# Optimization experiments

Hardware: AMD Instinct MI355X
Metric: run time of the kernel (lower is better)

Reference implementation:

```python
import jax, jax.numpy as jnp
import numpy as np

VALUE_RANGE = 16
D_MODEL = 1024
NUM_TILES = 8
NUM_FREQS = 6
BATCH = 65536
TEMPERATURE = 0.5


def _fourier(x):
    # x: (B,) -> (B, 2*NUM_FREQS); freqs = 2**[0..F)
    freqs = 2.0 ** jnp.arange(NUM_FREQS, dtype=jnp.float32)
    ang = x[:, None] * (2.0 * np.pi / VALUE_RANGE) * freqs[None, :]
    return jnp.concatenate([jnp.sin(ang), jnp.cos(ang)], axis=-1)


def _layernorm(x, g, b, eps=1e-5):
    m = jnp.mean(x, axis=-1, keepdims=True)
    v = jnp.var(x, axis=-1, keepdims=True)
    return (x - m) * jax.lax.rsqrt(v + eps) * g + b


def _gelu(x):
    return jax.nn.gelu(x, approximate=False)  # torch nn.GELU() default is exact erf


def setup_inputs() -> dict:
    key = jax.random.key(0)
    ks = jax.random.split(key, 16)
    d, T, F4 = D_MODEL, NUM_TILES, 4 * NUM_FREQS
    s = lambda i, shape, scale: (jax.random.normal(ks[i], shape, jnp.float32) * scale)
    return {
        "a": jax.random.uniform(ks[0], (BATCH,), jnp.float32, 0.0, float(VALUE_RANGE)),
        "b": jax.random.uniform(ks[1], (BATCH,), jnp.float32, 0.0, float(VALUE_RANGE)),
        "W_in": s(2, (F4, d), 0.05), "b_in": jnp.zeros((d,), jnp.float32),
        "ln_g": jnp.ones((d,), jnp.float32), "ln_b": jnp.zeros((d,), jnp.float32),
        "Wr1_sum": s(3, (d, d), 0.03), "br1_sum": jnp.zeros((d,), jnp.float32),
        "Wr2_sum": s(4, (d, T), 0.03), "br2_sum": jnp.zeros((T,), jnp.float32),
        "Wr1_diff": s(5, (d, d), 0.03), "br1_diff": jnp.zeros((d,), jnp.float32),
        "Wr2_diff": s(6, (d, T), 0.03), "br2_diff": jnp.zeros((T,), jnp.float32),
        "We1": s(7, (T, d, 2 * d), 0.03), "be1": jnp.zeros((T, 2 * d), jnp.float32),
        "We2": s(8, (T, 2 * d, d), 0.02), "be2": jnp.zeros((T, d), jnp.float32),
        "w_sum": s(9, (d,), 0.03), "bs": jnp.zeros((), jnp.float32),
        "w_diff": s(10, (d,), 0.03), "bd": jnp.zeros((), jnp.float32),
    }


def reference(a, b, W_in, b_in, ln_g, ln_b,
              Wr1_sum, br1_sum, Wr2_sum, br2_sum,
              Wr1_diff, br1_diff, Wr2_diff, br2_diff,
              We1, be1, We2, be2, w_sum, bs, w_diff, bd):
    # Shared encoder
    x = jnp.concatenate([_fourier(a), _fourier(b)], axis=-1)      # (B, 4F)
    x = _gelu(_layernorm(x @ W_in + b_in, ln_g, ln_b))            # (B, d)
    # Top-1 routing (temperature scaling does not change argmax, kept for fidelity)
    sum_logits = (_gelu(x @ Wr1_sum + br1_sum) @ Wr2_sum + br2_sum) / TEMPERATURE
    diff_logits = (_gelu(x @ Wr1_diff + br1_diff) @ Wr2_diff + br2_diff) / TEMPERATURE
    sum_tile = jnp.argmax(sum_logits, axis=-1)                    # (B,)
    diff_tile = jnp.argmax(diff_logits, axis=-1)                  # (B,)
    # Expert dispatch: loop over small fixed num_tiles, mask-combine per token.
    sum_hidden = jnp.zeros_like(x)
    diff_hidden = jnp.zeros_like(x)
    for t in range(We1.shape[0]):
        y = _gelu(x @ We1[t] + be1[t]) @ We2[t] + be2[t]          # (B, d)
        sum_hidden = sum_hidden + jnp.where((sum_tile == t)[:, None], y, 0.0)
        diff_hidden = diff_hidden + jnp.where((diff_tile == t)[:, None], y, 0.0)
    sum_pred = sum_hidden @ w_sum + bs                            # (B,)
    diff_pred = diff_hidden @ w_diff + bd                         # (B,)
    return (sum_pred, diff_pred)
```

## Files before the change

### kernel.cpp

```cpp
#include <hip/hip_runtime.h>
#include <math.h>


#define BT 65536
#define QN 65536
#define TSTR QN
#define D 1024
#define NT 8
#define DH 2048
#define RCAP 8192
#define RTOK 8
#define DELTA 0.010f
#define XJCAP 768

typedef _Float16 f16;
typedef _Float16 f16x8 __attribute__((ext_vector_type(8)));
typedef _Float16 f16x4 __attribute__((ext_vector_type(4)));
typedef float f32x16 __attribute__((ext_vector_type(16)));

__device__ __forceinline__ float gelu_f(float v) {
    return 0.5f * v * (1.0f + erff(v * 0.70710678118654752440f));
}

__device__ __forceinline__ float gelu_fast(float x) {
    float ax = fabsf(x) * 0.70710678118654752440f;
    float t = __builtin_amdgcn_rcpf(1.0f + 0.3275911f * ax);
    float p = t * (0.254829592f + t * (-0.284496736f + t * (1.421413741f +
              t * (-1.453152027f + t * 1.061405429f))));
    float er = 1.0f - p * __expf(-ax * ax);
    er = copysignf(er, x);
    return 0.5f * x * (1.0f + er);
}

__device__ __forceinline__ void gload16(const void* g, void* l) {
    __builtin_amdgcn_global_load_lds(
        (const __attribute__((address_space(1))) void*)g,
        (__attribute__((address_space(3))) void*)l, 16, 0, 0);
}

__global__ __launch_bounds__(256) void k_prev(
    const float* __restrict__ We2, const float* __restrict__ w_sum,
    const float* __restrict__ w_diff, const float* __restrict__ be2,
    const float* __restrict__ bs, const float* __restrict__ bd,
    float* __restrict__ v_sum, float* __restrict__ v_diff,
    float* __restrict__ c_sum, float* __restrict__ c_diff)
{
    int bid = blockIdx.x;
    if (bid < 4096) {
        int row  = bid * 4 + (threadIdx.x >> 6);
        int lane = threadIdx.x & 63;
        const float* r = We2 + (size_t)row * D;
        float s1 = 0.f, s2 = 0.f;
        #pragma unroll
        for (int i = 0; i < 4; i++) {
            int o4 = (lane + 64 * i) * 4;
            float4 w = *(const float4*)(r + o4);
            float4 u = *(const float4*)(w_sum + o4);
            float4 v = *(const float4*)(w_diff + o4);
            s1 += w.x*u.x + w.y*u.y + w.z*u.z + w.w*u.w;
            s2 += w.x*v.x + w.y*v.y + w.z*v.z + w.w*v.w;
        }
        #pragma unroll
        for (int m = 32; m >= 1; m >>= 1) {
            s1 += __shfl_xor(s1, m, 64);
            s2 += __shfl_xor(s2, m, 64);
        }
        if (lane == 0) { v_sum[row] = s1; v_diff[row] = s2; }
    } else {
        int t = threadIdx.x;
        if (t < 8) {
            float s = 0.f; const float* r = be2 + t * D;
            for (int k = 0; k < D; k++) s += r[k] * w_sum[k];
            c_sum[t] = s + bs[0];
        } else if (t < 16) {
            int tt = t - 8;
            float s = 0.f; const float* r = be2 + tt * D;
            for (int k = 0; k < D; k++) s += r[k] * w_diff[k];
            c_diff[tt] = s + bd[0];
        }
    }
}

__global__ __launch_bounds__(256) void k_cvt(
    const float* __restrict__ We1, f16* __restrict__ We1T)
{
    __shared__ float tile[64][65];
    int b = blockIdx.x;
    int e = b >> 9, rem = b & 511;
    int kt = rem >> 5, nt = rem & 31;
    int tid = threadIdx.x;
    const float* src = We1 + ((size_t)e * D + kt * 64) * DH + nt * 64;
    #pragma unroll
    for (int i = 0; i < 16; i++) {
        int idx = tid + 256 * i;
        int kk = idx >> 6, nn = idx & 63;
        tile[kk][nn] = src[(size_t)kk * DH + nn];
    }
    __syncthreads();
    f16* dst = We1T + ((size_t)e * DH + nt * 64) * D + kt * 64;
    #pragma unroll
    for (int i = 0; i < 16; i++) {
        int idx = tid + 256 * i;
        int nn = idx >> 6, kk = idx & 63;
        dst[(size_t)nn * D + kk] = (f16)tile[kk][nn];
    }
}

__global__ __launch_bounds__(256) void k_cvtR(
    const float* __restrict__ Wr1s, const float* __restrict__ Wr1d,
    f16* __restrict__ Wr1Tf)
{
    __shared__ float tile[64][65];
    int b = blockIdx.x;
    int z = b >> 8, rem = b & 255;
    int kt = rem >> 4, nt2 = rem & 15;
    int tid = threadIdx.x;
    const float* W = z ? Wr1d : Wr1s;
    const float* src = W + (size_t)(kt * 64) * 1024 + nt2 * 64;
    #pragma unroll
    for (int i = 0; i < 16; i++) {
        int idx = tid + 256 * i;
        int kk = idx >> 6, nn = idx & 63;
        tile[kk][nn] = src[(size_t)kk * 1024 + nn];
    }
    __syncthreads();
    f16* dst = Wr1Tf + (size_t)(z * 1024 + nt2 * 64) * 1024 + kt * 64;
    #pragma unroll
    for (int i = 0; i < 16; i++) {
        int idx = tid + 256 * i;
        int nn = idx >> 6, kk = idx & 63;
        dst[(size_t)nn * 1024 + kk] = (f16)tile[kk][nn];
    }
}

__global__ __launch_bounds__(256) void k_fuse(
    const float* __restrict__ br1s, const float* __restrict__ br1d,
    const float* __restrict__ Wr2s, const float* __restrict__ Wr2d,
    float* __restrict__ br1f, float* __restrict__ w2f)
{
    int tid = threadIdx.x;
    for (int n = tid; n < 2048; n += 256) {
        br1f[n] = (n < 1024) ? br1s[n] : br1d[n - 1024];
        const float* src = (n < 1024) ? (Wr2s + (size_t)n * 8)
                                      : (Wr2d + (size_t)(n - 1024) * 8);
        #pragma unroll
        for (int o = 0; o < 8; o++) w2f[(size_t)n * 8 + o] = src[o];
    }
}

__global__ __launch_bounds__(256) void k_enc(
    const float* __restrict__ a, const float* __restrict__ b,
    const float* __restrict__ W_in, const float* __restrict__ b_in,
    const float* __restrict__ ln_g, const float* __restrict__ ln_b,
    f16* __restrict__ xh)
{
    __shared__ float x0[64][24];
    __shared__ float red[8];
    int tid = threadIdx.x;
    float4 Wc[24];
    #pragma unroll
    for (int f = 0; f < 24; f++) Wc[f] = *(const float4*)(W_in + f * D + tid * 4);
    float4 bi = *(const float4*)(b_in + tid * 4);
    float4 gg = *(const float4*)(ln_g + tid * 4);
    float4 bb = *(const float4*)(ln_b + tid * 4);
    int base = blockIdx.x * 64;

    for (int idx = tid; idx < 64 * 12; idx += 256) {
        int t = idx / 12, q = idx - t * 12;
        int fr = q % 6;
        float in = (q < 6) ? a[base + t] : b[base + t];
        float ang = (in * 0.39269908169872414f) * (float)(1 << fr);
        int off = (q < 6) ? 0 : 12;
        x0[t][off + fr]     = sinf(ang);
        x0[t][off + 6 + fr] = cosf(ang);
    }
    __syncthreads();

    int lane = tid & 63, wid = tid >> 6;
    for (int t = 0; t < 64; t++) {
        float4 p = bi;
        #pragma unroll
        for (int f = 0; f < 24; f++) {
            float xv = x0[t][f];
            p.x += xv * Wc[f].x; p.y += xv * Wc[f].y;
            p.z += xv * Wc[f].z; p.w += xv * Wc[f].w;
        }
        float s1 = p.x + p.y + p.z + p.w;
        float s2 = p.x*p.x + p.y*p.y + p.z*p.z + p.w*p.w;
        #pragma unroll
        for (int m = 32; m >= 1; m >>= 1) {
            s1 += __shfl_xor(s1, m, 64);
            s2 += __shfl_xor(s2, m, 64);
        }
        if (lane == 0) { red[wid] = s1; red[4 + wid] = s2; }
        __syncthreads();
        float mean = (red[0] + red[1] + red[2] + red[3]) * (1.f / 1024.f);
        float ms   = (red[4] + red[5] + red[6] + red[7]) * (1.f / 1024.f);
        float inv  = 1.f / sqrtf(ms - mean * mean + 1e-5f);
        float4 o;
        o.x = gelu_f((p.x - mean) * inv * gg.x + bb.x);
        o.y = gelu_f((p.y - mean) * inv * gg.y + bb.y);
        o.z = gelu_f((p.z - mean) * inv * gg.z + bb.z);
        o.w = gelu_f((p.w - mean) * inv * gg.w + bb.w);
        size_t row = (size_t)(blockIdx.x * 64 + t);
        f16x4 h; h[0] = (f16)o.x; h[1] = (f16)o.y; h[2] = (f16)o.z; h[3] = (f16)o.w;
        *(f16x4*)(xh + row * D + tid * 4) = h;
        __syncthreads();
    }
}

__global__ __launch_bounds__(256, 3) void k_rtrm(
    const f16* __restrict__ xh, const f16* __restrict__ Wr1Tf,
    const float* __restrict__ br1f, const float* __restrict__ w2f,
    float* __restrict__ part)
{
    __shared__ char smem[40960] __attribute__((aligned(16)));
    int bid = blockIdx.x;
    int ntile = bid & 7;
    int ttile = bid >> 3;
    int tid = threadIdx.x;
    int lane = tid & 63, wid = tid >> 6;
    int hi = lane >> 5, l31 = lane & 31;
    int sg = tid >> 3, sc = tid & 7;

    const char* xb = (const char*)xh + (size_t)(ttile * 64) * 2048;
    const char* wb = (const char*)Wr1Tf + (size_t)(ntile * 256) * 2048;
    size_t goff = (size_t)sg * 2048 + (size_t)((sc * 16) ^ ((sg & 7) << 4));

    int axor = (l31 & 7) << 4;
    int kx[4];
    #pragma unroll
    for (int ks = 0; ks < 4; ks++) kx[ks] = (ks * 32 + hi * 16) ^ axor;
    int arow[2], brow[2];
    #pragma unroll
    for (int mi = 0; mi < 2; mi++) arow[mi] = (wid * 64 + mi * 32 + l31) * 128;
    #pragma unroll
    for (int ni = 0; ni < 2; ni++) brow[ni] = 32768 + (ni * 32 + l31) * 128;

    f32x16 acc[2][2];
    #pragma unroll
    for (int mi = 0; mi < 2; mi++)
        #pragma unroll
        for (int ni = 0; ni < 2; ni++) acc[mi][ni] = (f32x16)(0.0f);

    for (int k0 = 0; k0 < 1024; k0 += 64) {
        __syncthreads();
        #pragma unroll
        for (int i = 0; i < 8; i++)
            gload16(wb + (size_t)i * 32 * 2048 + k0 * 2 + goff,
                    smem + i * 4096 + wid * 1024);
        #pragma unroll
        for (int i = 0; i < 2; i++)
            gload16(xb + (size_t)i * 32 * 2048 + k0 * 2 + goff,
                    smem + 32768 + i * 4096 + wid * 1024);
        __syncthreads();
        #pragma unroll
        for (int ks = 0; ks < 4; ks++) {
            f16x8 a0 = *(const f16x8*)(smem + arow[0] + kx[ks]);
            f16x8 a1 = *(const f16x8*)(smem + arow[1] + kx[ks]);
            f16x8 b0 = *(const f16x8*)(smem + brow[0] + kx[ks]);
            f16x8 b1 = *(const f16x8*)(smem + brow[1] + kx[ks]);
            acc[0][0] = __builtin_amdgcn_mfma_f32_32x32x16_f16(a0, b0, acc[0][0], 0, 0, 0);
            acc[0][1] = __builtin_amdgcn_mfma_f32_32x32x16_f16(a0, b1, acc[0][1], 0, 0, 0);
            acc[1][0] = __builtin_amdgcn_mfma_f32_32x32x16_f16(a1, b0, acc[1][0], 0, 0, 0);
            acc[1][1] = __builtin_amdgcn_mfma_f32_32x32x16_f16(a1, b1, acc[1][1], 0, 0, 0);
        }
    }

    float lp[2][8] = {};
    #pragma unroll
    for (int mi = 0; mi < 2; mi++) {
        #pragma unroll
        for (int r = 0; r < 16; r++) {
            int nl = wid * 64 + mi * 32 + (r & 3) + 8 * (r >> 2) + 4 * hi;
            int gn = ntile * 256 + nl;
            float b1 = br1f[gn];
            float4 wa = *(const float4*)(w2f + (size_t)gn * 8);
            float4 wc = *(const float4*)(w2f + (size_t)gn * 8 + 4);
            float h0 = gelu_fast(acc[mi][0][r] + b1);
            float h1 = gelu_fast(acc[mi][1][r] + b1);
            lp[0][0] += h0*wa.x; lp[0][1] += h0*wa.y;
            lp[0][2] += h0*wa.z; lp[0][3] += h0*wa.w;
            lp[0][4] += h0*wc.x; lp[0][5] += h0*wc.y;
            lp[0][6] += h0*wc.z; lp[0][7] += h0*wc.w;
            lp[1][0] += h1*wa.x; lp[1][1] += h1*wa.y;
            lp[1][2] += h1*wa.z; lp[1][3] += h1*wa.w;
            lp[1][4] += h1*wc.x; lp[1][5] += h1*wc.y;
            lp[1][6] += h1*wc.z; lp[1][7] += h1*wc.w;
        }
    }
    #pragma unroll
    for (int ni = 0; ni < 2; ni++)
        #pragma unroll
        for (int o = 0; o < 8; o++)
            lp[ni][o] += __shfl_xor(lp[ni][o], 32, 64);
    __syncthreads();
    float* redf = (float*)smem;
    if (hi == 0) {
        #pragma unroll
        for (int ni = 0; ni < 2; ni++)
            #pragma unroll
            for (int o = 0; o < 8; o++)
                redf[(wid * 64 + ni * 32 + l31) * 8 + o] = lp[ni][o];
    }
    __syncthreads();
    for (int idx = tid; idx < 512; idx += 256) {
        int tok = idx >> 3, o = idx & 7;
        float s = ((redf[(0 * 64 + tok) * 8 + o]  + redf[(1 * 64 + tok) * 8 + o])
                 +  redf[(2 * 64 + tok) * 8 + o]) + redf[(3 * 64 + tok) * 8 + o];
        part[((size_t)(ttile * 64 + tok) * 8 + ntile) * 8 + o] = s;
    }
}

__device__ __forceinline__ void emit_tasks(int tok, int ts, int td,
                                           int* tasks, int* cnts)
{
    if (ts == td) {
        int s = atomicAdd(&cnts[ts], 1);
        tasks[ts * TSTR + s] = tok | (3 << 17);
    } else {
        int s1 = atomicAdd(&cnts[ts], 1);
        tasks[ts * TSTR + s1] = tok | (1 << 17);
        int s2 = atomicAdd(&cnts[td], 1);
        tasks[td * TSTR + s2] = tok | (2 << 17);
    }
}

__global__ __launch_bounds__(256) void k_amx2(
    const float* __restrict__ part, const float* __restrict__ b2s,
    const float* __restrict__ b2d, int* __restrict__ tasks,
    int* __restrict__ ctrl, int* __restrict__ redoS, int* __restrict__ redoD)
{
    int i = blockIdx.x * 256 + threadIdx.x;
    const float* p = part + (size_t)i * 64;
    float Ls[8], Ld[8];
    #pragma unroll
    for (int o = 0; o < 8; o++) { Ls[o] = b2s[o]; Ld[o] = b2d[o]; }
    #pragma unroll
    for (int nt = 0; nt < 4; nt++)
        #pragma unroll
        for (int o = 0; o < 8; o++) Ls[o] += p[nt * 8 + o];
    #pragma unroll
    for (int nt = 4; nt < 8; nt++)
        #pragma unroll
        for (int o = 0; o < 8; o++) Ld[o] += p[nt * 8 + o];

    int as = 0; float m1s = Ls[0];
    #pragma unroll
    for (int o = 1; o < 8; o++) if (Ls[o] > m1s) { m1s = Ls[o]; as = o; }
    float m2s = -1e30f;
    #pragma unroll
    for (int o = 0; o < 8; o++) if (o != as && Ls[o] > m2s) m2s = Ls[o];
    int ad = 0; float m1d = Ld[0];
    #pragma unroll
    for (int o = 1; o < 8; o++) if (Ld[o] > m1d) { m1d = Ld[o]; ad = o; }
    float m2d = -1e30f;
    #pragma unroll
    for (int o = 0; o < 8; o++) if (o != ad && Ld[o] > m2d) m2d = Ld[o];

    bool sM = (m1s - m2s) < DELTA;
    bool dM = (m1d - m2d) < DELTA;
    if (!sM && !dM) { emit_tasks(i, as, ad, tasks, ctrl); return; }
    int posS = -1, posD = -1;
    if (sM) { posS = atomicAdd(&ctrl[8], 1); if (posS >= RCAP) { sM = false; posS = -1; } }
    if (dM) { posD = atomicAdd(&ctrl[9], 1); if (posD >= RCAP) { dM = false; posD = -1; } }
    if (!sM && !dM) { emit_tasks(i, as, ad, tasks, ctrl); return; }
    if (sM) redoS[posS] = i | (ad << 17) | ((dM ? 1 : 0) << 20);
    if (dM) redoD[posD] = i | (as << 17) | ((sM ? 1 : 0) << 20);
}

__global__ __launch_bounds__(256) void k_redo(
    const float* __restrict__ a, const float* __restrict__ b,
    const float* __restrict__ W_in, const float* __restrict__ b_in,
    const float* __restrict__ ln_g, const float* __restrict__ ln_b,
    const float* __restrict__ Wr1s, const float* __restrict__ br1s,
    const float* __restrict__ Wr2s,
    const float* __restrict__ Wr1d, const float* __restrict__ br1d,
    const float* __restrict__ Wr2d,
    const int* __restrict__ redoS, const int* __restrict__ redoD,
    const int* __restrict__ ctrl,
    float* __restrict__ rlogpS, float* __restrict__ rlogpD)
{
    int z = blockIdx.y;
    int rcnt = min(ctrl[8 + z], RCAP);
    int s0 = blockIdx.x * RTOK;
    if (s0 >= rcnt) return;
    const int* list = z ? redoD : redoS;
    const float* Wr1 = z ? Wr1d : Wr1s;
    const float* br1v = z ? br1d : br1s;
    const float* Wr2 = z ? Wr2d : Wr2s;

    __shared__ float xl[RTOK][1024];
    __shared__ float x0[RTOK][24];
    __shared__ float wred[4][RTOK][2];
    __shared__ float lred[4][RTOK][8];
    __shared__ int tokR[RTOK];
    int tid = threadIdx.x;
    int lane = tid & 63, wid = tid >> 6;

    if (tid < RTOK) tokR[tid] = list[min(s0 + tid, rcnt - 1)] & 0xFFFF;
    __syncthreads();

    if (tid < RTOK * 12) {
        int t = tid / 12, q = tid - t * 12;
        int fr = q % 6;
        int tok = tokR[t];
        float in = (q < 6) ? a[tok] : b[tok];
        float ang = (in * 0.39269908169872414f) * (float)(1 << fr);
        int off = (q < 6) ? 0 : 12;
        x0[t][off + fr]     = sinf(ang);
        x0[t][off + 6 + fr] = cosf(ang);
    }
    __syncthreads();

    {
        float4 Wc[24];
        #pragma unroll
        for (int f = 0; f < 24; f++) Wc[f] = *(const float4*)(W_in + f * D + tid * 4);
        float4 bi = *(const float4*)(b_in + tid * 4);
        float4 gg = *(const float4*)(ln_g + tid * 4);
        float4 bb = *(const float4*)(ln_b + tid * 4);
        float p[RTOK][4];
        #pragma unroll
        for (int r = 0; r < RTOK; r++) {
            float4 pv = bi;
            #pragma unroll
            for (int f = 0; f < 24; f++) {
                float xv = x0[r][f];
                pv.x += xv * Wc[f].x; pv.y += xv * Wc[f].y;
                pv.z += xv * Wc[f].z; pv.w += xv * Wc[f].w;
            }
            p[r][0] = pv.x; p[r][1] = pv.y; p[r][2] = pv.z; p[r][3] = pv.w;
            float s1 = pv.x + pv.y + pv.z + pv.w;
            float s2 = pv.x*pv.x + pv.y*pv.y + pv.z*pv.z + pv.w*pv.w;
            #pragma unroll
            for (int m = 32; m >= 1; m >>= 1) {
                s1 += __shfl_xor(s1, m, 64);
                s2 += __shfl_xor(s2, m, 64);
            }
            if (lane == 0) { wred[wid][r][0] = s1; wred[wid][r][1] = s2; }
        }
        __syncthreads();
        #pragma unroll
        for (int r = 0; r < RTOK; r++) {
            float mean = (wred[0][r][0] + wred[1][r][0] + wred[2][r][0] + wred[3][r][0]) * (1.f / 1024.f);
            float ms   = (wred[0][r][1] + wred[1][r][1] + wred[2][r][1] + wred[3][r][1]) * (1.f / 1024.f);
            float inv  = 1.f / sqrtf(ms - mean * mean + 1e-5f);
            float gv[4] = {gg.x, gg.y, gg.z, gg.w};
            float bv[4] = {bb.x, bb.y, bb.z, bb.w};
            #pragma unroll
            for (int jj = 0; jj < 4; jj++)
                xl[r][tid * 4 + jj] = gelu_f((p[r][jj] - mean) * inv * gv[jj] + bv[jj]);
        }
    }
    __syncthreads();

    int c0 = tid * 4;
    float hacc[RTOK][4] = {};
    #pragma unroll 4
    for (int k = 0; k < 1024; k++) {
        float4 wv = *(const float4*)(Wr1 + (size_t)k * 1024 + c0);
        #pragma unroll
        for (int r = 0; r < RTOK; r++) {
            float xv = xl[r][k];
            hacc[r][0] += xv * wv.x; hacc[r][1] += xv * wv.y;
            hacc[r][2] += xv * wv.z; hacc[r][3] += xv * wv.w;
        }
    }
    float L[RTOK][8] = {};
    #pragma unroll
    for (int jj = 0; jj < 4; jj++) {
        int col = c0 + jj;
        float b1 = br1v[col];
        float4 wa = *(const float4*)(Wr2 + (size_t)col * 8);
        float4 wc = *(const float4*)(Wr2 + (size_t)col * 8 + 4);
        #pragma unroll
        for (int r = 0; r < RTOK; r++) {
            float h = gelu_f(hacc[r][jj] + b1);
            L[r][0] += h*wa.x; L[r][1] += h*wa.y; L[r][2] += h*wa.z; L[r][3] += h*wa.w;
            L[r][4] += h*wc.x; L[r][5] += h*wc.y; L[r][6] += h*wc.z; L[r][7] += h*wc.w;
        }
    }
    #pragma unroll
    for (int m = 32; m >= 1; m >>= 1)
        #pragma unroll
        for (int r = 0; r < RTOK; r++)
            #pragma unroll
            for (int o = 0; o < 8; o++)
                L[r][o] += __shfl_xor(L[r][o], m, 64);
    if (lane == 0) {
        #pragma unroll
        for (int r = 0; r < RTOK; r++)
            #pragma unroll
            for (int o = 0; o < 8; o++)
                lred[wid][r][o] = L[r][o];
    }
    __syncthreads();
    if (tid < RTOK * 8) {
        int r = tid >> 3, o = tid & 7;
        int slot = s0 + r;
        if (slot < rcnt) {
            float v = ((lred[0][r][o] + lred[1][r][o]) + lred[2][r][o]) + lred[3][r][o];
            float* dst = z ? rlogpD : rlogpS;
            dst[(size_t)slot * 8 + o] = v;
        }
    }
}

__global__ __launch_bounds__(256) void k_amx3d(
    const float* __restrict__ rlogpD, const int* __restrict__ redoD,
    const float* __restrict__ b2d, int* __restrict__ tasks,
    int* __restrict__ ctrl, int* __restrict__ adx)
{
    int rcnt = min(ctrl[9], RCAP);
    for (int s = blockIdx.x * 256 + threadIdx.x; s < rcnt; s += gridDim.x * 256) {
        int entry = redoD[s];
        int tok = entry & 0xFFFF;
        float L[8];
        #pragma unroll
        for (int o = 0; o < 8; o++) L[o] = rlogpD[(size_t)s * 8 + o] + b2d[o];
        int td = 0; float bv = L[0];
        #pragma unroll
        for (int o = 1; o < 8; o++) if (L[o] > bv) { bv = L[o]; td = o; }
        adx[tok] = td;
        if (!((entry >> 20) & 1))
            emit_tasks(tok, (entry >> 17) & 7, td, tasks, ctrl);
    }
}

__global__ __launch_bounds__(256) void k_amx3s(
    const float* __restrict__ rlogpS, const int* __restrict__ redoS,
    const float* __restrict__ b2s, int* __restrict__ tasks,
    int* __restrict__ ctrl, const int* __restrict__ adx)
{
    int rcnt = min(ctrl[8], RCAP);
    for (int s = blockIdx.x * 256 + threadIdx.x; s < rcnt; s += gridDim.x * 256) {
        int entry = redoS[s];
        int tok = entry & 0xFFFF;
        float L[8];
        #pragma unroll
        for (int o = 0; o < 8; o++) L[o] = rlogpS[(size_t)s * 8 + o] + b2s[o];
        int ts = 0; float bv = L[0];
        #pragma unroll
        for (int o = 1; o < 8; o++) if (L[o] > bv) { bv = L[o]; ts = o; }
        int td = ((entry >> 20) & 1) ? adx[tok] : ((entry >> 17) & 7);
        emit_tasks(tok, ts, td, tasks, ctrl);
    }
}

__global__ void k_sched(const int* __restrict__ ctrl, int* __restrict__ xjob)
{
    __shared__ int seg[17];
    __shared__ int Jt[2];
    int tid = threadIdx.x;
    if (tid == 0) {
        int o = 0;
        for (int e = 0; e < 8; e++) {
            int nt2 = (ctrl[e] + 127) >> 7;
            seg[e * 2]     = o; o += nt2;
            seg[e * 2 + 1] = o; o += nt2;
        }
        seg[16] = o;
        Jt[0] = o; Jt[1] = (o + 7) >> 3;
    }
    __syncthreads();
    int J = Jt[0], target = Jt[1];
    for (int g = tid; g < J; g += blockDim.x) {
        int s = 0;
        while (s < 15 && seg[s + 1] <= g) s++;
        int e = s >> 1, ch = s & 1, rt = g - seg[s];
        int x = g / target; if (x > 7) x = 7;
        int pos = g - x * target;
        xjob[x * XJCAP + pos] = e | (ch << 3) | (rt << 4);
    }
    if (tid < 8) {
        int c = J - tid * target;
        if (c < 0) c = 0;
        if (c > target) c = target;
        xjob[8 * XJCAP + tid] = c;
    }
}

__global__ __launch_bounds__(256) void k_expm(
    const f16* __restrict__ xh, const f16* __restrict__ We1T,
    const float* __restrict__ be1, const float* __restrict__ v_sum,
    const float* __restrict__ v_diff, const float* __restrict__ c_sum,
    const float* __restrict__ c_diff, const int* __restrict__ tasks,
    const int* __restrict__ counts, const int* __restrict__ xjob,
    float* __restrict__ ppS, float* __restrict__ ppD)
{
    int xcd  = blockIdx.x & 7;
    int slot = blockIdx.x >> 3;
    int nj = xjob[8 * XJCAP + xcd];

    __shared__ char smem[49152] __attribute__((aligned(16)));
    __shared__ int tokL[128];
    __shared__ int flgL[128];
    __shared__ float redS[2][128];
    __shared__ float redD[2][128];

    int tid = threadIdx.x;
    int lane = tid & 63;
    int wid  = tid >> 6;
    int wr = wid >> 1, wc = wid & 1;
    int hi = lane >> 5, l31 = lane & 31;
    int sg = tid >> 3, sc = tid & 7;
    int goffc = (sc * 16) ^ ((sg & 7) << 4);

    const char* xh_b = (const char*)xh;

    int axor = (l31 & 7) << 4;
    int kx[4];
    #pragma unroll
    for (int ks = 0; ks < 4; ks++) kx[ks] = (ks * 32 + hi * 16) ^ axor;
    int arow[2], nrow[4];
    #pragma unroll
    for (int mi = 0; mi < 2; mi++) arow[mi] = (wr * 64 + mi * 32 + l31) * 128;
    #pragma unroll
    for (int ni = 0; ni < 4; ni++) nrow[ni] = 16384 + (wc * 128 + ni * 32 + l31) * 128;

    for (int j = slot; j < nj; j += 256) {
        int jv = xjob[xcd * XJCAP + j];
        int e  = jv & 7;
        int ch = (jv >> 3) & 1;
        int rt = jv >> 4;
        int cnt = counts[e];
        int r0 = rt * 128;
        const char* bbase = (const char*)(We1T + (size_t)e * DH * D);

        __syncthreads();
        if (tid < 128) {
            int idx = r0 + tid;
            int tv = tasks[e * TSTR + min(idx, cnt - 1)];
            tokL[tid] = tv & 0xFFFF;
            flgL[tid] = (idx < cnt) ? ((tv >> 17) & 3) : 0;
        }
        {
            int w2 = tid >> 7, row = tid & 127;
            redS[w2][row] = 0.f;
            redD[w2][row] = 0.f;
        }
        __syncthreads();
        size_t asrc[4];
        #pragma unroll
        for (int i = 0; i < 4; i++)
            asrc[i] = (size_t)tokL[i * 32 + sg] * 2048 + goffc;

        for (int nt = 0; nt < 4; ++nt) {
            int n0 = ch * 1024 + nt * 256;
            f32x16 acc[2][4];
            #pragma unroll
            for (int mi = 0; mi < 2; mi++)
                #pragma unroll
                for (int ni = 0; ni < 4; ni++) acc[mi][ni] = (f32x16)(0.0f);
            const char* bs0 = bbase + ((size_t)n0 + sg) * 2048 + goffc;

            for (int k0b = 0; k0b < 2048; k0b += 128) {
                __syncthreads();
                #pragma unroll
                for (int i = 0; i < 4; i++)
                    gload16(xh_b + asrc[i] + k0b, smem + i * 4096 + wid * 1024);
                #pragma unroll
                for (int i = 0; i < 8; i++)
                    gload16(bs0 + (size_t)i * 32 * 2048 + k0b,
                            smem + 16384 + i * 4096 + wid * 1024);
                __syncthreads();
                #pragma unroll
                for (int ks = 0; ks < 4; ks++) {
                    f16x8 a0 = *(const f16x8*)(smem + arow[0] + kx[ks]);
                    f16x8 a1 = *(const f16x8*)(smem + arow[1] + kx[ks]);
                    #pragma unroll
                    for (int ni = 0; ni < 4; ni++) {
                        f16x8 bf = *(const f16x8*)(smem + nrow[ni] + kx[ks]);
                        acc[0][ni] = __builtin_amdgcn_mfma_f32_32x32x16_f16(a0, bf, acc[0][ni], 0, 0, 0);
                        acc[1][ni] = __builtin_amdgcn_mfma_f32_32x32x16_f16(a1, bf, acc[1][ni], 0, 0, 0);
                    }
                }
            }
            #pragma unroll
            for (int mi = 0; mi < 2; mi++) {
                float hs[16], hd[16];
                #pragma unroll
                for (int r = 0; r < 16; r++) { hs[r] = 0.f; hd[r] = 0.f; }
                #pragma unroll
                for (int ni = 0; ni < 4; ni++) {
                    int col = n0 + wc * 128 + ni * 32 + l31;
                    float b1 = be1[e * DH + col];
                    float vs = v_sum[(size_t)e * DH + col];
                    float vd = v_diff[(size_t)e * DH + col];
                    #pragma unroll
                    for (int r = 0; r < 16; r++) {
                        float h = gelu_fast(acc[mi][ni][r] + b1);
                        hs[r] += h * vs;
                        hd[r] += h * vd;
                    }
                }
                #pragma unroll
                for (int m = 16; m >= 1; m >>= 1) {
                    #pragma unroll
                    for (int r = 0; r < 16; r++) {
                        hs[r] += __shfl_xor(hs[r], m, 64);
                        hd[r] += __shfl_xor(hd[r], m, 64);
                    }
                }
                if (l31 == 0) {
                    #pragma unroll
                    for (int r = 0; r < 16; r++) {
                        int row = wr * 64 + mi * 32 + (r & 3) + 8 * (r >> 2) + 4 * hi;
                        redS[wc][row] += hs[r];
                        redD[wc][row] += hd[r];
                    }
                }
            }
        }

        __syncthreads();
        if (tid < 128) {
            int idx = r0 + tid;
            if (idx < cnt) {
                int fl = flgL[tid];
                int tok = tokL[tid];
                float s = redS[0][tid] + redS[1][tid];
                float d = redD[0][tid] + redD[1][tid];
                if (ch == 0) { s += c_sum[e]; d += c_diff[e]; }
                if (fl & 1) ppS[ch * QN + tok] = s;
                if (fl & 2) ppD[ch * QN + tok] = d;
            }
        }
    }
}

__global__ __launch_bounds__(256) void k_fin(
    const float* __restrict__ ppS, const float* __restrict__ ppD,
    float* __restrict__ out)
{
    int i = blockIdx.x * 256 + threadIdx.x;
    out[i]      = ppS[i] + ppS[QN + i];
    out[BT + i] = ppD[i] + ppD[QN + i];
}

extern "C" void kernel_launch(void* const* d_in, const int* in_sizes, int n_in,
                              void* d_out, int out_size, void* d_ws, size_t ws_size,
                              hipStream_t stream)
{
    const float* a      = (const float*)d_in[0];
    const float* b      = (const float*)d_in[1];
    const float* W_in   = (const float*)d_in[2];
    const float* b_in   = (const float*)d_in[3];
    const float* ln_g   = (const float*)d_in[4];
    const float* ln_b   = (const float*)d_in[5];
    const float* Wr1s   = (const float*)d_in[6];
    const float* br1s   = (const float*)d_in[7];
    const float* Wr2s   = (const float*)d_in[8];
    const float* br2s   = (const float*)d_in[9];
    const float* Wr1d   = (const float*)d_in[10];
    const float* br1d   = (const float*)d_in[11];
    const float* Wr2d   = (const float*)d_in[12];
    const float* br2d   = (const float*)d_in[13];
    const float* We1    = (const float*)d_in[14];
    const float* be1    = (const float*)d_in[15];
    const float* We2    = (const float*)d_in[16];
    const float* be2    = (const float*)d_in[17];
    const float* w_sum  = (const float*)d_in[18];
    const float* bs     = (const float*)d_in[19];
    const float* w_diff = (const float*)d_in[20];
    const float* bd     = (const float*)d_in[21];
    float* out = (float*)d_out;

    char* w = (char*)d_ws;
    size_t off = 0;
    auto alloc = [&](size_t bytes) -> char* {
        char* p = w + off;
        off = (off + bytes + 255) & ~(size_t)255;
        return p;
    };
    float* v_sum   = (float*)alloc((size_t)NT * DH * 4);
    float* v_diff  = (float*)alloc((size_t)NT * DH * 4);
    float* c_sum   = (float*)alloc(64);
    float* c_diff  = (float*)alloc(64);
    f16*   xh      = (f16*)alloc((size_t)QN * D * 2);
    float* part    = (float*)alloc((size_t)QN * 64 * 4);
    float* rlogpS  = (float*)alloc((size_t)RCAP * 8 * 4);
    float* rlogpD  = (float*)alloc((size_t)RCAP * 8 * 4);
    int*   redoS   = (int*)alloc((size_t)RCAP * 4);
    int*   redoD   = (int*)alloc((size_t)RCAP * 4);
    int*   adx     = (int*)alloc((size_t)QN * 4);
    int*   tasks   = (int*)alloc((size_t)NT * QN * 4);
    int*   ctrl    = (int*)alloc(64);
    int*   xjob    = (int*)alloc((size_t)(8 * XJCAP + 8) * 4);
    float* ppS     = (float*)alloc((size_t)2 * QN * 4);
    float* ppD     = (float*)alloc((size_t)2 * QN * 4);
    f16*   We1T    = (f16*)alloc((size_t)NT * DH * D * 2);
    f16*   Wr1Tf   = (f16*)alloc((size_t)2048 * 1024 * 2);
    float* br1f    = (float*)alloc((size_t)2048 * 4);
    float* w2f     = (float*)alloc((size_t)2048 * 8 * 4);
    if (off > ws_size) {
        hipMemsetAsync(d_out, 0, (size_t)out_size * 4, stream);
        return;
    }

    k_cvt <<<dim3(4096), dim3(256), 0, stream>>>(We1, We1T);
    k_cvtR<<<dim3(512),  dim3(256), 0, stream>>>(Wr1s, Wr1d, Wr1Tf);
    k_fuse<<<dim3(1),    dim3(256), 0, stream>>>(br1s, br1d, Wr2s, Wr2d, br1f, w2f);
    k_prev<<<dim3(4097), dim3(256), 0, stream>>>(We2, w_sum, w_diff, be2, bs, bd,
                                                 v_sum, v_diff, c_sum, c_diff);
    k_enc<<<dim3(QN / 64), dim3(256), 0, stream>>>(a, b, W_in, b_in, ln_g, ln_b, xh);
    k_rtrm<<<dim3(QN / 64 * 8), dim3(256), 0, stream>>>(xh, Wr1Tf, br1f, w2f, part);
    hipMemsetAsync(ctrl, 0, 64, stream);
    k_amx2<<<dim3(QN / 256), dim3(256), 0, stream>>>(part, br2s, br2d, tasks, ctrl,
                                                     redoS, redoD);
    k_redo<<<dim3(RCAP / RTOK, 2), dim3(256), 0, stream>>>(
        a, b, W_in, b_in, ln_g, ln_b,
        Wr1s, br1s, Wr2s, Wr1d, br1d, Wr2d,
        redoS, redoD, ctrl, rlogpS, rlogpD);
    k_amx3d<<<dim3(16), dim3(256), 0, stream>>>(rlogpD, redoD, br2d, tasks, ctrl, adx);
    k_amx3s<<<dim3(16), dim3(256), 0, stream>>>(rlogpS, redoS, br2s, tasks, ctrl, adx);
    k_sched<<<dim3(1), dim3(256), 0, stream>>>(ctrl, xjob);
    k_expm<<<dim3(2048), dim3(256), 0, stream>>>(xh, We1T, be1, v_sum, v_diff,
                                                 c_sum, c_diff, tasks, ctrl, xjob,
                                                 ppS, ppD);
    k_fin<<<dim3(QN / 256), dim3(256), 0, stream>>>(ppS, ppD, out);
}
```

Measured before the change: 2.657 ms.

## Merge expert hidden-dim halves into one job and batch encoder layernorm syncs

The expert kernel no longer splits the 2048-wide hidden dimension into two jobs. Each job now loops over all eight 256-column chunks and writes the final sum/diff predictions straight to the output, which removes the partial-sum buffers and the separate finalize kernel. The schedule is simplified to match. Separately, the encoder processes eight tokens per barrier pair instead of one, cutting __syncthreads count in the layernorm reduction. The trade-offs are half as many expert jobs, so less parallelism, and more registers in the encoder.

```diff
diff --git a/kernel.cpp b/kernel.cpp
--- a/kernel.cpp
+++ b/kernel.cpp
@@ -155,7 +155,7 @@
     f16* __restrict__ xh)
 {
     __shared__ float x0[64][24];
-    __shared__ float red[8];
+    __shared__ float red[4][8][2];
     int tid = threadIdx.x;
     float4 Wc[24];
     #pragma unroll
@@ -177,34 +177,43 @@
     __syncthreads();
 
     int lane = tid & 63, wid = tid >> 6;
-    for (int t = 0; t < 64; t++) {
-        float4 p = bi;
-        #pragma unroll
-        for (int f = 0; f < 24; f++) {
-            float xv = x0[t][f];
-            p.x += xv * Wc[f].x; p.y += xv * Wc[f].y;
-            p.z += xv * Wc[f].z; p.w += xv * Wc[f].w;
-        }
-        float s1 = p.x + p.y + p.z + p.w;
-        float s2 = p.x*p.x + p.y*p.y + p.z*p.z + p.w*p.w;
-        #pragma unroll
-        for (int m = 32; m >= 1; m >>= 1) {
-            s1 += __shfl_xor(s1, m, 64);
-            s2 += __shfl_xor(s2, m, 64);
-        }
-        if (lane == 0) { red[wid] = s1; red[4 + wid] = s2; }
+    for (int t8 = 0; t8 < 8; t8++) {
+        float p[8][4];
+        #pragma unroll
+        for (int tt = 0; tt < 8; tt++) {
+            int t = t8 * 8 + tt;
+            float4 pv = bi;
+            #pragma unroll
+            for (int f = 0; f < 24; f++) {
+                float xv = x0[t][f];
+                pv.x += xv * Wc[f].x; pv.y += xv * Wc[f].y;
+                pv.z += xv * Wc[f].z; pv.w += xv * Wc[f].w;
+            }
+            p[tt][0] = pv.x; p[tt][1] = pv.y; p[tt][2] = pv.z; p[tt][3] = pv.w;
+            float s1 = pv.x + pv.y + pv.z + pv.w;
+            float s2 = pv.x*pv.x + pv.y*pv.y + pv.z*pv.z + pv.w*pv.w;
+            #pragma unroll
+            for (int m = 32; m >= 1; m >>= 1) {
+                s1 += __shfl_xor(s1, m, 64);
+                s2 += __shfl_xor(s2, m, 64);
+            }
+            if (lane == 0) { red[wid][tt][0] = s1; red[wid][tt][1] = s2; }
+        }
         __syncthreads();
-        float mean = (red[0] + red[1] + red[2] + red[3]) * (1.f / 1024.f);
-        float ms   = (red[4] + red[5] + red[6] + red[7]) * (1.f / 1024.f);
-        float inv  = 1.f / sqrtf(ms - mean * mean + 1e-5f);
-        float4 o;
-        o.x = gelu_f((p.x - mean) * inv * gg.x + bb.x);
-        o.y = gelu_f((p.y - mean) * inv * gg.y + bb.y);
-        o.z = gelu_f((p.z - mean) * inv * gg.z + bb.z);
-        o.w = gelu_f((p.w - mean) * inv * gg.w + bb.w);
-        size_t row = (size_t)(blockIdx.x * 64 + t);
-        f16x4 h; h[0] = (f16)o.x; h[1] = (f16)o.y; h[2] = (f16)o.z; h[3] = (f16)o.w;
-        *(f16x4*)(xh + row * D + tid * 4) = h;
+        #pragma unroll
+        for (int tt = 0; tt < 8; tt++) {
+            int t = t8 * 8 + tt;
+            float mean = (red[0][tt][0] + red[1][tt][0] + red[2][tt][0] + red[3][tt][0]) * (1.f / 1024.f);
+            float ms   = (red[0][tt][1] + red[1][tt][1] + red[2][tt][1] + red[3][tt][1]) * (1.f / 1024.f);
+            float inv  = 1.f / sqrtf(ms - mean * mean + 1e-5f);
+            float o0 = gelu_f((p[tt][0] - mean) * inv * gg.x + bb.x);
+            float o1 = gelu_f((p[tt][1] - mean) * inv * gg.y + bb.y);
+            float o2 = gelu_f((p[tt][2] - mean) * inv * gg.z + bb.z);
+            float o3 = gelu_f((p[tt][3] - mean) * inv * gg.w + bb.w);
+            size_t row = (size_t)(blockIdx.x * 64 + t);
+            f16x4 h; h[0] = (f16)o0; h[1] = (f16)o1; h[2] = (f16)o2; h[3] = (f16)o3;
+            *(f16x4*)(xh + row * D + tid * 4) = h;
+        }
         __syncthreads();
     }
 }
@@ -550,28 +559,27 @@
 
 __global__ void k_sched(const int* __restrict__ ctrl, int* __restrict__ xjob)
 {
-    __shared__ int seg[17];
+    __shared__ int seg[9];
     __shared__ int Jt[2];
     int tid = threadIdx.x;
     if (tid == 0) {
         int o = 0;
         for (int e = 0; e < 8; e++) {
-            int nt2 = (ctrl[e] + 127) >> 7;
-            seg[e * 2]     = o; o += nt2;
-            seg[e * 2 + 1] = o; o += nt2;
-        }
-        seg[16] = o;
+            seg[e] = o;
+            o += (ctrl[e] + 127) >> 7;
+        }
+        seg[8] = o;
         Jt[0] = o; Jt[1] = (o + 7) >> 3;
     }
     __syncthreads();
     int J = Jt[0], target = Jt[1];
     for (int g = tid; g < J; g += blockDim.x) {
         int s = 0;
-        while (s < 15 && seg[s + 1] <= g) s++;
-        int e = s >> 1, ch = s & 1, rt = g - seg[s];
+        while (s < 7 && seg[s + 1] <= g) s++;
+        int e = s, rt = g - seg[s];
         int x = g / target; if (x > 7) x = 7;
         int pos = g - x * target;
-        xjob[x * XJCAP + pos] = e | (ch << 3) | (rt << 4);
+        xjob[x * XJCAP + pos] = e | (rt << 4);
     }
     if (tid < 8) {
         int c = J - tid * target;
@@ -587,7 +595,7 @@
     const float* __restrict__ v_diff, const float* __restrict__ c_sum,
     const float* __restrict__ c_diff, const int* __restrict__ tasks,
     const int* __restrict__ counts, const int* __restrict__ xjob,
-    float* __restrict__ ppS, float* __restrict__ ppD)
+    float* __restrict__ out)
 {
     int xcd  = blockIdx.x & 7;
     int slot = blockIdx.x >> 3;
@@ -622,7 +630,6 @@
     for (int j = slot; j < nj; j += 256) {
         int jv = xjob[xcd * XJCAP + j];
         int e  = jv & 7;
-        int ch = (jv >> 3) & 1;
         int rt = jv >> 4;
         int cnt = counts[e];
         int r0 = rt * 128;
@@ -646,8 +653,8 @@
         for (int i = 0; i < 4; i++)
             asrc[i] = (size_t)tokL[i * 32 + sg] * 2048 + goffc;
 
-        for (int nt = 0; nt < 4; ++nt) {
-            int n0 = ch * 1024 + nt * 256;
+        for (int nt = 0; nt < 8; ++nt) {
+            int n0 = nt * 256;
             f32x16 acc[2][4];
             #pragma unroll
             for (int mi = 0; mi < 2; mi++)
@@ -720,23 +727,13 @@
             if (idx < cnt) {
                 int fl = flgL[tid];
                 int tok = tokL[tid];
-                float s = redS[0][tid] + redS[1][tid];
-                float d = redD[0][tid] + redD[1][tid];
-                if (ch == 0) { s += c_sum[e]; d += c_diff[e]; }
-                if (fl & 1) ppS[ch * QN + tok] = s;
-                if (fl & 2) ppD[ch * QN + tok] = d;
+                float s = (redS[0][tid] + redS[1][tid]) + c_sum[e];
+                float d = (redD[0][tid] + redD[1][tid]) + c_diff[e];
+                if (fl & 1) out[tok] = s;
+                if (fl & 2) out[BT + tok] = d;
             }
         }
     }
-}
-
-__global__ __launch_bounds__(256) void k_fin(
-    const float* __restrict__ ppS, const float* __restrict__ ppD,
-    float* __restrict__ out)
-{
-    int i = blockIdx.x * 256 + threadIdx.x;
-    out[i]      = ppS[i] + ppS[QN + i];
-    out[BT + i] = ppD[i] + ppD[QN + i];
 }
 
 extern "C" void kernel_launch(void* const* d_in, const int* in_sizes, int n_in,
@@ -788,8 +785,6 @@
     int*   tasks   = (int*)alloc((size_t)NT * QN * 4);
     int*   ctrl    = (int*)alloc(64);
     int*   xjob    = (int*)alloc((size_t)(8 * XJCAP + 8) * 4);
-    float* ppS     = (float*)alloc((size_t)2 * QN * 4);
-    float* ppD     = (float*)alloc((size_t)2 * QN * 4);
     f16*   We1T    = (f16*)alloc((size_t)NT * DH * D * 2);
     f16*   Wr1Tf   = (f16*)alloc((size_t)2048 * 1024 * 2);
     float* br1f    = (float*)alloc((size_t)2048 * 4);
@@ -817,7 +812,5 @@
     k_amx3s<<<dim3(16), dim3(256), 0, stream>>>(rlogpS, redoS, br2s, tasks, ctrl, adx);
     k_sched<<<dim3(1), dim3(256), 0, stream>>>(ctrl, xjob);
     k_expm<<<dim3(2048), dim3(256), 0, stream>>>(xh, We1T, be1, v_sum, v_diff,
-                                                 c_sum, c_diff, tasks, ctrl, xjob,
-                                                 ppS, ppD);
-    k_fin<<<dim3(QN / 256), dim3(256), 0, stream>>>(ppS, ppD, out);
-}
+                                                 c_sum, c_diff, tasks, ctrl, xjob, out);
+}
```

Result: slower. 2.716 ms (+2.2%).
